# Performance work log

Hardware: AMD Instinct MI355X
Metric: run time of the kernel (lower is better)

The kernel has to match this reference:

```python
import jax, jax.numpy as jnp
import numpy as np

D_MODEL = 1024
NHEAD = 16
D_K = D_MODEL // NHEAD
EPS_ATTN = 1e-6
EPS_LN = 1e-5


def _linear(k, fan_in, fan_out):
    k1, k2 = jax.random.split(k)
    bound = 1.0 / np.sqrt(fan_in)
    W = jax.random.uniform(k1, (fan_out, fan_in), jnp.float32, -bound, bound)
    b = jax.random.uniform(k2, (fan_out,), jnp.float32, -bound, bound)
    return W, b


def setup_inputs() -> dict:
    key = jax.random.key(0)
    ks = jax.random.split(key, 8)
    src = jax.random.normal(ks[0], (4096, 4, D_MODEL), jnp.float32)
    Wq, bq = _linear(ks[1], D_MODEL, D_MODEL)
    Wk, bk = _linear(ks[2], D_MODEL, D_MODEL)
    Wv, bv = _linear(ks[3], D_MODEL, D_MODEL)
    Wo, bo = _linear(ks[4], D_MODEL, D_MODEL)
    W1, b1 = _linear(ks[5], D_MODEL, 2 * D_MODEL)
    W2, b2 = _linear(ks[6], 2 * D_MODEL, D_MODEL)
    g1 = jnp.ones((D_MODEL,), jnp.float32)
    be1 = jnp.zeros((D_MODEL,), jnp.float32)
    g2 = jnp.ones((D_MODEL,), jnp.float32)
    be2 = jnp.zeros((D_MODEL,), jnp.float32)
    return {"src": src, "Wq": Wq, "bq": bq, "Wk": Wk, "bk": bk, "Wv": Wv, "bv": bv,
            "Wo": Wo, "bo": bo, "W1": W1, "b1": b1, "W2": W2, "b2": b2,
            "g1": g1, "be1": be1, "g2": g2, "be2": be2}


def _layernorm(x, g, b):
    mu = jnp.mean(x, axis=-1, keepdims=True)
    var = jnp.mean(jnp.square(x - mu), axis=-1, keepdims=True)
    return (x - mu) * jax.lax.rsqrt(var + EPS_LN) * g + b


def reference(src, Wq, bq, Wk, bk, Wv, bv, Wo, bo, W1, b1, W2, b2, g1, be1, g2, be2):
    S, B, D = src.shape
    Q = src @ Wq.T + bq  # [S,B,D]
    K = src @ Wk.T + bk
    V = src @ Wv.T + bv
    # split heads: [S,B,H,dk]
    Q = Q.reshape(S, B, NHEAD, D_K)
    K = K.reshape(S, B, NHEAD, D_K)
    V = V.reshape(S, B, NHEAD, D_K)
    phiQ = jax.nn.elu(Q) + 1.0
    phiK = jax.nn.elu(K) + 1.0
    # context per (batch, head): [B,H,dk,dk]
    context = jnp.einsum('sbhd,sbhe->bhde', phiK, V)
    out = jnp.einsum('sbhd,bhde->sbhe', phiQ, context)
    denom = jnp.einsum('sbhd,bhd->sbh', phiQ, phiK.sum(axis=0))
    out = out / (denom[..., None] + EPS_ATTN)
    attn = out.reshape(S, B, D)  # concat heads
    out = attn @ Wo.T + bo  # dropout = identity (eval)
    out = _layernorm(src + out, g1, be1)
    ffn = jax.nn.relu(out @ W1.T + b1) @ W2.T + b2
    out = _layernorm(out + ffn, g2, be2)
    return out
```

## Files before the change

kernel.cpp:

```cpp
#include <hip/hip_runtime.h>
#include <hip/hip_bf16.h>

typedef __hip_bfloat16 bf16;
typedef __attribute__((ext_vector_type(4))) float floatx4;
typedef __attribute__((ext_vector_type(8))) short shortx8;

#define MFMA16(a, b, c) __builtin_amdgcn_mfma_f32_16x16x32_bf16(a, b, c, 0, 0, 0)

__device__ __forceinline__ void gll16(const bf16* g, void* l) {
  __builtin_amdgcn_global_load_lds((const __attribute__((address_space(1))) unsigned int*)g,
                                   (__attribute__((address_space(3))) unsigned int*)l,
                                   16, 0, 0);
}

__device__ __forceinline__ shortx8 ds8(const char* p) {
  shortx8 r;
  unsigned a = (unsigned)(unsigned long long)(const __attribute__((address_space(3))) char*)p;
  asm volatile("ds_read_b128 %0, %1" : "=v"(r) : "v"(a));
  return r;
}

__device__ __forceinline__ float b2f(short s) {
  return __bfloat162float(__builtin_bit_cast(bf16, (unsigned short)s));
}
__device__ __forceinline__ short f2b(float f) {
  return __builtin_bit_cast(short, __float2bfloat16(f));
}

__global__ __launch_bounds__(256) void f2b_all(
    const float* __restrict__ src, const float* __restrict__ Wq,
    const float* __restrict__ Wk, const float* __restrict__ Wv,
    const float* __restrict__ Wo, const float* __restrict__ W1,
    const float* __restrict__ W2, bf16* __restrict__ src_bf,
    bf16* __restrict__ Wq_b, bf16* __restrict__ Wk_b, bf16* __restrict__ Wv_b,
    bf16* __restrict__ Wo_b, bf16* __restrict__ W1_b, bf16* __restrict__ W2_b) {
  const int blk = blockIdx.x;
  const float* in;
  bf16* out;
  int off;
  if (blk < 16384)      { in = src; out = src_bf; off = blk; }
  else if (blk < 17408) { in = Wq; out = Wq_b; off = blk - 16384; }
  else if (blk < 18432) { in = Wk; out = Wk_b; off = blk - 17408; }
  else if (blk < 19456) { in = Wv; out = Wv_b; off = blk - 18432; }
  else if (blk < 20480) { in = Wo; out = Wo_b; off = blk - 19456; }
  else if (blk < 22528) { in = W1; out = W1_b; off = blk - 20480; }
  else                  { in = W2; out = W2_b; off = blk - 22528; }
  const int i = (off * 256 + threadIdx.x) * 4;
  float4 v = *(const float4*)(in + i);
  ushort4 u;
  u.x = (unsigned short)f2b(v.x);
  u.y = (unsigned short)f2b(v.y);
  u.z = (unsigned short)f2b(v.z);
  u.w = (unsigned short)f2b(v.w);
  *(ushort4*)(out + i) = u;
}

template <int EPI>
__global__ __launch_bounds__(512, 2) void gemm256(
    const bf16* __restrict__ A, const bf16* __restrict__ Bw,
    const float* __restrict__ bias0, const float* __restrict__ bias1,
    const float* __restrict__ bias2, const float* __restrict__ resf,
    const bf16* __restrict__ resb, void* __restrict__ out0,
    void* __restrict__ out1, void* __restrict__ out2, const int M,
    const int K) {
  __shared__ __align__(16) char smem[131072];
  const int tid = threadIdx.x;
  const int lane = tid & 63, wave = tid >> 6;
  const int wm = wave & 1, wn = wave >> 1;
  const int bm = blockIdx.x, bn = blockIdx.y;
  const int NK = K >> 5;

  const int srow = tid >> 2;
  const int schunk = (tid & 3) ^ ((srow >> 1) & 3);
  const bf16* gA0 = A + (size_t)(bm * 256 + srow) * K + schunk * 8;
  const bf16* gA1 = gA0 + (size_t)128 * K;
  const bf16* gB0 = Bw + (size_t)(bn * 256 + srow) * K + schunk * 8;
  const bf16* gB1 = gB0 + (size_t)128 * K;
  const unsigned ldst = (unsigned)wave * 1024u;

  const int frow = lane & 15;
  const unsigned fch16 = (unsigned)(((lane >> 4) ^ ((frow >> 1) & 3))) << 4;
  const unsigned aoff0 = (unsigned)(wm * 8192 + frow * 64) + fch16;
  const unsigned boff0 = 65536u + (unsigned)(wn * 4096 + frow * 64) + fch16;

  floatx4 acc[8][4] = {};

#define STAGE_A(t)                                                       \
  {                                                                      \
    const int kk = (t) * 32;                                             \
    const unsigned bo = (unsigned)(((t) & 3) * 16384) + ldst;            \
    gll16(gA0 + kk, smem + bo);                                          \
    gll16(gA1 + kk, smem + bo + 8192);                                   \
  }
#define STAGE_B(t)                                                       \
  {                                                                      \
    const int kk = (t) * 32;                                             \
    const unsigned bo = 65536u + (unsigned)(((t) & 3) * 16384) + ldst;   \
    gll16(gB0 + kk, smem + bo);                                          \
    gll16(gB1 + kk, smem + bo + 8192);                                   \
  }

  STAGE_A(0); STAGE_B(0);
  STAGE_A(1); STAGE_B(1);
  STAGE_A(2); STAGE_B(2);
  asm volatile("s_waitcnt vmcnt(8)");
  __builtin_amdgcn_sched_barrier(0);
  __builtin_amdgcn_s_barrier();

  for (int kt = 0; kt < NK; ++kt) {
    const unsigned ab = aoff0 + (unsigned)((kt & 3) * 16384);
    const unsigned bb = boff0 + (unsigned)((kt & 3) * 16384);
    shortx8 bfr[4], af[4];
#pragma unroll
    for (int j = 0; j < 4; j++) bfr[j] = ds8(smem + bb + j * 1024);
#pragma unroll
    for (int i2 = 0; i2 < 4; i2++) af[i2] = ds8(smem + ab + i2 * 1024);
    if (kt + 3 < NK) STAGE_A(kt + 3);
    __builtin_amdgcn_s_barrier();
    asm volatile("s_waitcnt lgkmcnt(0)");
    __builtin_amdgcn_sched_barrier(0);
    __builtin_amdgcn_s_setprio(1);
#pragma unroll
    for (int i2 = 0; i2 < 4; i2++)
#pragma unroll
      for (int j = 0; j < 4; j++) acc[i2][j] = MFMA16(af[i2], bfr[j], acc[i2][j]);
    __builtin_amdgcn_s_setprio(0);
#pragma unroll
    for (int i2 = 0; i2 < 4; i2++) af[i2] = ds8(smem + ab + (4 + i2) * 1024);
    if (kt + 3 < NK) STAGE_B(kt + 3);
    __builtin_amdgcn_s_barrier();
    asm volatile("s_waitcnt lgkmcnt(0)");
    __builtin_amdgcn_sched_barrier(0);
    __builtin_amdgcn_s_setprio(1);
#pragma unroll
    for (int i2 = 0; i2 < 4; i2++)
#pragma unroll
      for (int j = 0; j < 4; j++)
        acc[4 + i2][j] = MFMA16(af[i2], bfr[j], acc[4 + i2][j]);
    __builtin_amdgcn_s_setprio(0);
    if (kt < NK - 1) {
      if (kt < NK - 3) {
        asm volatile("s_waitcnt vmcnt(8)");
      } else if (kt == NK - 3) {
        asm volatile("s_waitcnt vmcnt(4)");
      } else {
        asm volatile("s_waitcnt vmcnt(0)");
      }
      __builtin_amdgcn_sched_barrier(0);
      __builtin_amdgcn_s_barrier();
    }
  }
#undef STAGE_A
#undef STAGE_B

  bf16* cep = (bf16*)smem;
  const float* bptr = bias0;
  bf16* ob = (bf16*)out0;
  int colbase = bn * 256;
  int phi = 0;
  if (EPI == 4) {
    const int sel = bn >> 2;
    bptr = (sel == 0) ? bias0 : (sel == 1) ? bias1 : bias2;
    ob = (bf16*)((sel == 0) ? out0 : (sel == 1) ? out1 : out2);
    colbase = (bn & 3) * 256;
    phi = (sel < 2);
  }
  const int e = lane & 15, q4 = (lane >> 4) << 2;
  float bj[4];
#pragma unroll
  for (int j = 0; j < 4; j++) bj[j] = bptr[colbase + wn * 64 + j * 16 + e];

  const int ridx = tid >> 4;
  const int cc = (tid & 15) * 8;
  const int grow_base = bm * 256 + (ridx >> 4) * 128 + (ridx & 15);

#pragma unroll
  for (int i3 = 0; i3 < 8; i3++) {
    __syncthreads();
#pragma unroll
    for (int j = 0; j < 4; j++)
#pragma unroll
      for (int r = 0; r < 4; r++) {
        float v = acc[i3][j][r] + bj[j];
        if (EPI == 4 && phi) v = v > 0.f ? v + 1.f : __expf(v);
        if (EPI == 2) v = fmaxf(v, 0.f);
        cep[(wm * 16 + q4 + r) * 268 + wn * 64 + j * 16 + e] =
            __builtin_bit_cast(bf16, f2b(v));
      }
    __syncthreads();
    const int grow = grow_base + i3 * 16;
#pragma unroll
    for (int h = 0; h < 2; h++) {
      const int col = cc + h * 128;
      shortx8 v = *(const shortx8*)&cep[ridx * 268 + col];
      if (EPI == 3) {
        const float* rp = resf + (size_t)grow * M + colbase + col;
        float4 r0 = *(const float4*)rp;
        float4 r1 = *(const float4*)(rp + 4);
        v[0] = f2b(b2f(v[0]) + r0.x); v[1] = f2b(b2f(v[1]) + r0.y);
        v[2] = f2b(b2f(v[2]) + r0.z); v[3] = f2b(b2f(v[3]) + r0.w);
        v[4] = f2b(b2f(v[4]) + r1.x); v[5] = f2b(b2f(v[5]) + r1.y);
        v[6] = f2b(b2f(v[6]) + r1.z); v[7] = f2b(b2f(v[7]) + r1.w);
      } else if (EPI == 5) {
        shortx8 rv = *(const shortx8*)(resb + (size_t)grow * M + colbase + col);
#pragma unroll
        for (int k = 0; k < 8; k++) v[k] = f2b(b2f(v[k]) + b2f(rv[k]));
      }
      *(shortx8*)(ob + (size_t)grow * M + colbase + col) = v;
    }
  }
}

__global__ __launch_bounds__(256) void ctx_mfma(const bf16* __restrict__ phiK,
                                                const bf16* __restrict__ V,
                                                float* __restrict__ ctx,
                                                float* __restrict__ ksum) {
  __shared__ __align__(16) short sKT[64][72];
  __shared__ __align__(16) short sVT[64][72];
  const int bh = blockIdx.x, b = bh >> 4, h = bh & 15;
  const int t = threadIdx.x, lane = t & 63, wave = t >> 6;
  const int s_l = t >> 2;
  const int c0 = (t & 3) << 4;
  const int frow = lane & 15, fk = (lane >> 4) << 3;
  const shortx8 ones = (shortx8)(short)0x3F80;
  floatx4 acc[4] = {};
  floatx4 accK = {};

  const int sbeg = blockIdx.y * 512;
  for (int sub = 0; sub < 8; sub++) {
    const size_t g = ((size_t)(sbeg + sub * 64 + s_l) * 4 + b) * 1024 + h * 64 + c0;
    shortx8 kv0 = *(const shortx8*)(phiK + g);
    shortx8 kv1 = *(const shortx8*)(phiK + g + 8);
    shortx8 vv0 = *(const shortx8*)(V + g);
    shortx8 vv1 = *(const shortx8*)(V + g + 8);
    __syncthreads();
#pragma unroll
    for (int j = 0; j < 8; j++) {
      sKT[c0 + j][s_l] = kv0[j];
      sKT[c0 + 8 + j][s_l] = kv1[j];
      sVT[c0 + j][s_l] = vv0[j];
      sVT[c0 + 8 + j][s_l] = vv1[j];
    }
    __syncthreads();
#pragma unroll
    for (int ks = 0; ks < 2; ks++) {
      shortx8 af = *(const shortx8*)&sKT[wave * 16 + frow][ks * 32 + fk];
      accK = MFMA16(af, ones, accK);
#pragma unroll
      for (int j = 0; j < 4; j++) {
        shortx8 bfr = *(const shortx8*)&sVT[j * 16 + frow][ks * 32 + fk];
        acc[j] = MFMA16(af, bfr, acc[j]);
      }
    }
  }

  float* cdst = ctx + (size_t)bh * 4096;
  const int dr0 = wave * 16 + ((lane >> 4) << 2);
  const int e = lane & 15;
#pragma unroll
  for (int j = 0; j < 4; j++)
#pragma unroll
    for (int r = 0; r < 4; r++)
      atomicAdd(cdst + (size_t)(dr0 + r) * 64 + j * 16 + e, acc[j][r]);
  if (e == 0) {
#pragma unroll
    for (int r = 0; r < 4; r++) atomicAdd(ksum + bh * 64 + dr0 + r, accK[r]);
  }
}

__global__ __launch_bounds__(256) void attn_mfma(const bf16* __restrict__ phiQ,
                                                 const float* __restrict__ ctx,
                                                 const float* __restrict__ ksum,
                                                 bf16* __restrict__ attn) {
  __shared__ __align__(16) bf16 sctxT[64][72];
  __shared__ __align__(16) bf16 sks[64];
  const int bh = blockIdx.x, b = bh >> 4, h = bh & 15;
  const int t = threadIdx.x, lane = t & 63, wave = t >> 6;
  const float* cbase = ctx + (size_t)bh * 4096;
  for (int idx = t; idx < 4096; idx += 256) {
    int d = idx >> 6, e = idx & 63;
    sctxT[e][d] = __float2bfloat16(cbase[idx]);
  }
  if (t < 64) sks[t] = __float2bfloat16(ksum[bh * 64 + t]);
  __syncthreads();

  const int s0 = blockIdx.y * 128 + wave * 32;
  const int frow = lane & 15, fk = (lane >> 4) << 3;
  shortx8 bfr[2][4], kfr[2];
#pragma unroll
  for (int ks = 0; ks < 2; ks++) {
#pragma unroll
    for (int j = 0; j < 4; j++) bfr[ks][j] = *(const shortx8*)&sctxT[j * 16 + frow][ks * 32 + fk];
    kfr[ks] = *(const shortx8*)&sks[ks * 32 + fk];
  }
  floatx4 acc[2][4] = {};
  floatx4 accd[2] = {};
#pragma unroll
  for (int i = 0; i < 2; i++) {
#pragma unroll
    for (int ks = 0; ks < 2; ks++) {
      const int srow = s0 + i * 16 + frow;
      const bf16* ap = phiQ + ((size_t)srow * 4 + b) * 1024 + h * 64 + ks * 32 + fk;
      shortx8 af = *(const shortx8*)ap;
#pragma unroll
      for (int j = 0; j < 4; j++) acc[i][j] = MFMA16(af, bfr[ks][j], acc[i][j]);
      accd[i] = MFMA16(af, kfr[ks], accd[i]);
    }
  }
#pragma unroll
  for (int i = 0; i < 2; i++) {
#pragma unroll
    for (int r = 0; r < 4; r++) {
      const int srow = s0 + i * 16 + ((lane >> 4) << 2) + r;
      const float den = accd[i][r] + 1e-6f;
#pragma unroll
      for (int j = 0; j < 4; j++) {
        const int e = j * 16 + (lane & 15);
        attn[((size_t)srow * 4 + b) * 1024 + h * 64 + e] = __float2bfloat16(acc[i][j][r] / den);
      }
    }
  }
}

__global__ __launch_bounds__(256) void ln_kernel(const bf16* __restrict__ x,
                                                 const float* __restrict__ g,
                                                 const float* __restrict__ be,
                                                 bf16* __restrict__ outb,
                                                 float* __restrict__ outf) {
  const int row = blockIdx.x, t = threadIdx.x;
  const ushort4 u = ((const ushort4*)(x + (size_t)row * 1024))[t];
  float v0 = b2f((short)u.x), v1 = b2f((short)u.y);
  float v2 = b2f((short)u.z), v3 = b2f((short)u.w);
  float s = v0 + v1 + v2 + v3;
  float q = v0 * v0 + v1 * v1 + v2 * v2 + v3 * v3;
#pragma unroll
  for (int off = 32; off; off >>= 1) {
    s += __shfl_xor(s, off);
    q += __shfl_xor(q, off);
  }
  __shared__ float ss[4], sq[4];
  const int wave = t >> 6;
  if ((t & 63) == 0) { ss[wave] = s; sq[wave] = q; }
  __syncthreads();
  s = ss[0] + ss[1] + ss[2] + ss[3];
  q = sq[0] + sq[1] + sq[2] + sq[3];
  const float mu = s * (1.f / 1024.f);
  const float var = q * (1.f / 1024.f) - mu * mu;
  const float rstd = rsqrtf(var + 1e-5f);
  const float4 gv = ((const float4*)g)[t];
  const float4 bv = ((const float4*)be)[t];
  float y0 = (v0 - mu) * rstd * gv.x + bv.x;
  float y1 = (v1 - mu) * rstd * gv.y + bv.y;
  float y2 = (v2 - mu) * rstd * gv.z + bv.z;
  float y3 = (v3 - mu) * rstd * gv.w + bv.w;
  if (outb != nullptr) {
    ushort4 o;
    o.x = (unsigned short)f2b(y0); o.y = (unsigned short)f2b(y1);
    o.z = (unsigned short)f2b(y2); o.w = (unsigned short)f2b(y3);
    ((ushort4*)(outb + (size_t)row * 1024))[t] = o;
  } else {
    float4 o = {y0, y1, y2, y3};
    ((float4*)(outf + (size_t)row * 1024))[t] = o;
  }
}

extern "C" void kernel_launch(void* const* d_in, const int* in_sizes, int n_in,
                              void* d_out, int out_size, void* d_ws, size_t ws_size,
                              hipStream_t stream) {
  const float* src = (const float*)d_in[0];
  const float* Wq = (const float*)d_in[1];
  const float* bq = (const float*)d_in[2];
  const float* Wk = (const float*)d_in[3];
  const float* bk = (const float*)d_in[4];
  const float* Wv = (const float*)d_in[5];
  const float* bv = (const float*)d_in[6];
  const float* Wo = (const float*)d_in[7];
  const float* bo = (const float*)d_in[8];
  const float* W1 = (const float*)d_in[9];
  const float* b1 = (const float*)d_in[10];
  const float* W2 = (const float*)d_in[11];
  const float* b2 = (const float*)d_in[12];
  const float* g1 = (const float*)d_in[13];
  const float* be1 = (const float*)d_in[14];
  const float* g2 = (const float*)d_in[15];
  const float* be2 = (const float*)d_in[16];

  const size_t MB = 1024 * 1024;
  char* w = (char*)d_ws;
  bf16* src_bf = (bf16*)(w + 0);
  bf16* x1b = (bf16*)(w + 0);
  bf16* phiQ = (bf16*)(w + 64 * MB);
  bf16* phiK = (bf16*)(w + 96 * MB);
  bf16* attn = (bf16*)(w + 96 * MB);
  bf16* Vb = (bf16*)(w + 128 * MB);
  bf16* out1b = (bf16*)(w + 128 * MB);
  bf16* x2b = (bf16*)(w + 160 * MB);
  bf16* Wq_b = (bf16*)(w + 224 * MB);
  bf16* Wk_b = (bf16*)(w + 226 * MB);
  bf16* Wv_b = (bf16*)(w + 228 * MB);
  bf16* Wo_b = (bf16*)(w + 230 * MB);
  bf16* W1_b = (bf16*)(w + 232 * MB);
  bf16* W2_b = (bf16*)(w + 236 * MB);
  float* ctx = (float*)(w + 240 * MB);
  float* ksum = (float*)(w + 241 * MB);
  bf16* H1 = (bf16*)d_out;
  float* outf = (float*)d_out;

  const dim3 blk(256), blk5(512);
  f2b_all<<<24576, blk, 0, stream>>>(src, Wq, Wk, Wv, Wo, W1, W2, src_bf, Wq_b,
                                     Wk_b, Wv_b, Wo_b, W1_b, W2_b);
  hipMemsetAsync(ctx, 0, (64 * 64 * 64 + 64 * 64) * sizeof(float), stream);

  gemm256<4><<<dim3(64, 12), blk5, 0, stream>>>(
      src_bf, Wq_b, bq, bk, bv, nullptr, nullptr, phiQ, phiK, Vb, 1024, 1024);
  ctx_mfma<<<dim3(64, 8), blk, 0, stream>>>(phiK, Vb, ctx, ksum);
  attn_mfma<<<dim3(64, 32), blk, 0, stream>>>(phiQ, ctx, ksum, attn);
  gemm256<3><<<dim3(64, 4), blk5, 0, stream>>>(
      attn, Wo_b, bo, nullptr, nullptr, src, nullptr, x1b, nullptr, nullptr, 1024, 1024);
  ln_kernel<<<16384, blk, 0, stream>>>(x1b, g1, be1, out1b, nullptr);
  gemm256<2><<<dim3(64, 8), blk5, 0, stream>>>(
      out1b, W1_b, b1, nullptr, nullptr, nullptr, nullptr, H1, nullptr, nullptr, 2048, 1024);
  gemm256<5><<<dim3(64, 4), blk5, 0, stream>>>(
      H1, W2_b, b2, nullptr, nullptr, nullptr, out1b, x2b, nullptr, nullptr, 1024, 2048);
  ln_kernel<<<16384, blk, 0, stream>>>(x2b, g2, be2, nullptr, outf);
}
```

Before: 531.8 us.

## Add double-buffered BK=64 GEMM variant for the Wo and FFN projections

Introduces a second GEMM kernel that stages 64-wide K tiles into two LDS buffers of 64KB each with XOR-swizzled chunks, using a simpler one-barrier-per-tile loop. It is used for the output projection and both FFN GEMMs, while the original multi-stage kernel (renamed) stays for the QKV projection. The aim is fewer barriers and less loop overhead per K step, at the cost of shallower prefetch depth, which may expose more global load latency.

```diff
diff --git a/kernel.cpp b/kernel.cpp
--- a/kernel.cpp
+++ b/kernel.cpp
@@ -56,7 +56,7 @@
 }
 
 template <int EPI>
-__global__ __launch_bounds__(512, 2) void gemm256(
+__global__ __launch_bounds__(512, 2) void gemm_p2(
     const bf16* __restrict__ A, const bf16* __restrict__ Bw,
     const float* __restrict__ bias0, const float* __restrict__ bias1,
     const float* __restrict__ bias2, const float* __restrict__ resf,
@@ -152,6 +152,136 @@
   }
 #undef STAGE_A
 #undef STAGE_B
+
+  bf16* cep = (bf16*)smem;
+  const float* bptr = bias0;
+  bf16* ob = (bf16*)out0;
+  int colbase = bn * 256;
+  int phi = 0;
+  if (EPI == 4) {
+    const int sel = bn >> 2;
+    bptr = (sel == 0) ? bias0 : (sel == 1) ? bias1 : bias2;
+    ob = (bf16*)((sel == 0) ? out0 : (sel == 1) ? out1 : out2);
+    colbase = (bn & 3) * 256;
+    phi = (sel < 2);
+  }
+  const int e = lane & 15, q4 = (lane >> 4) << 2;
+  float bj[4];
+#pragma unroll
+  for (int j = 0; j < 4; j++) bj[j] = bptr[colbase + wn * 64 + j * 16 + e];
+
+  const int ridx = tid >> 4;
+  const int cc = (tid & 15) * 8;
+  const int grow_base = bm * 256 + (ridx >> 4) * 128 + (ridx & 15);
+
+#pragma unroll
+  for (int i3 = 0; i3 < 8; i3++) {
+    __syncthreads();
+#pragma unroll
+    for (int j = 0; j < 4; j++)
+#pragma unroll
+      for (int r = 0; r < 4; r++) {
+        float v = acc[i3][j][r] + bj[j];
+        if (EPI == 4 && phi) v = v > 0.f ? v + 1.f : __expf(v);
+        if (EPI == 2) v = fmaxf(v, 0.f);
+        cep[(wm * 16 + q4 + r) * 268 + wn * 64 + j * 16 + e] =
+            __builtin_bit_cast(bf16, f2b(v));
+      }
+    __syncthreads();
+    const int grow = grow_base + i3 * 16;
+#pragma unroll
+    for (int h = 0; h < 2; h++) {
+      const int col = cc + h * 128;
+      shortx8 v = *(const shortx8*)&cep[ridx * 268 + col];
+      if (EPI == 3) {
+        const float* rp = resf + (size_t)grow * M + colbase + col;
+        float4 r0 = *(const float4*)rp;
+        float4 r1 = *(const float4*)(rp + 4);
+        v[0] = f2b(b2f(v[0]) + r0.x); v[1] = f2b(b2f(v[1]) + r0.y);
+        v[2] = f2b(b2f(v[2]) + r0.z); v[3] = f2b(b2f(v[3]) + r0.w);
+        v[4] = f2b(b2f(v[4]) + r1.x); v[5] = f2b(b2f(v[5]) + r1.y);
+        v[6] = f2b(b2f(v[6]) + r1.z); v[7] = f2b(b2f(v[7]) + r1.w);
+      } else if (EPI == 5) {
+        shortx8 rv = *(const shortx8*)(resb + (size_t)grow * M + colbase + col);
+#pragma unroll
+        for (int k = 0; k < 8; k++) v[k] = f2b(b2f(v[k]) + b2f(rv[k]));
+      }
+      *(shortx8*)(ob + (size_t)grow * M + colbase + col) = v;
+    }
+  }
+}
+
+template <int EPI>
+__global__ __launch_bounds__(512, 2) void gemm_mb(
+    const bf16* __restrict__ A, const bf16* __restrict__ Bw,
+    const float* __restrict__ bias0, const float* __restrict__ bias1,
+    const float* __restrict__ bias2, const float* __restrict__ resf,
+    const bf16* __restrict__ resb, void* __restrict__ out0,
+    void* __restrict__ out1, void* __restrict__ out2, const int M,
+    const int K) {
+  __shared__ __align__(16) char smem[131072];
+  const int tid = threadIdx.x;
+  const int lane = tid & 63, wave = tid >> 6;
+  const int wm = wave & 1, wn = wave >> 1;
+  const int bm = blockIdx.x, bn = blockIdx.y;
+  const int NT = K >> 6;
+
+  const int srow = tid >> 3;
+  const int sch = (tid & 7) ^ (srow & 7);
+  const bf16* gA0 = A + (size_t)(bm * 256 + srow) * K + sch * 8;
+  const bf16* gB0 = Bw + (size_t)(bn * 256 + srow) * K + sch * 8;
+  const unsigned ldst = (unsigned)wave * 1024u;
+
+  const int frow = lane & 15, lq = lane >> 4, x7 = frow & 7;
+  const unsigned arow = (unsigned)(wm * 128 + frow) * 128u;
+  const unsigned brow = 32768u + (unsigned)(wn * 64 + frow) * 128u;
+  const unsigned aoffA = arow + (unsigned)((lq ^ x7) * 16);
+  const unsigned aoffB = arow + (unsigned)(((4 | lq) ^ x7) * 16);
+  const unsigned boffA = brow + (unsigned)((lq ^ x7) * 16);
+  const unsigned boffB = brow + (unsigned)(((4 | lq) ^ x7) * 16);
+
+  floatx4 acc[8][4] = {};
+
+#define STAGE(t)                                                           \
+  {                                                                        \
+    const int kk = (t) * 64;                                               \
+    const unsigned so2 = (unsigned)(((t) & 1) * 65536);                    \
+    gll16(gA0 + kk, smem + so2 + ldst);                                    \
+    gll16(gA0 + (size_t)64 * K + kk, smem + so2 + 8192 + ldst);            \
+    gll16(gA0 + (size_t)128 * K + kk, smem + so2 + 16384 + ldst);          \
+    gll16(gA0 + (size_t)192 * K + kk, smem + so2 + 24576 + ldst);          \
+    gll16(gB0 + kk, smem + so2 + 32768 + ldst);                            \
+    gll16(gB0 + (size_t)64 * K + kk, smem + so2 + 40960 + ldst);           \
+    gll16(gB0 + (size_t)128 * K + kk, smem + so2 + 49152 + ldst);          \
+    gll16(gB0 + (size_t)192 * K + kk, smem + so2 + 57344 + ldst);          \
+  }
+
+  STAGE(0);
+  __syncthreads();
+
+  for (int kt = 0; kt < NT; ++kt) {
+    const unsigned so = (unsigned)((kt & 1) * 65536);
+    if (kt + 1 < NT) STAGE(kt + 1);
+    shortx8 af[8], bfr[4];
+#pragma unroll
+    for (int ks = 0; ks < 2; ks++) {
+      const unsigned ao = so + (ks ? aoffB : aoffA);
+      const unsigned bo = so + (ks ? boffB : boffA);
+#pragma unroll
+      for (int j = 0; j < 4; j++)
+        bfr[j] = *(const shortx8*)(smem + bo + j * 2048);
+#pragma unroll
+      for (int i = 0; i < 8; i++)
+        af[i] = *(const shortx8*)(smem + ao + i * 2048);
+#pragma unroll
+      for (int i = 0; i < 8; i++)
+#pragma unroll
+        for (int j = 0; j < 4; j++)
+          acc[i][j] = MFMA16(af[i], bfr[j], acc[i][j]);
+    }
+    __syncthreads();
+  }
+#undef STAGE
 
   bf16* cep = (bf16*)smem;
   const float* bptr = bias0;
@@ -411,16 +541,16 @@
                                      Wk_b, Wv_b, Wo_b, W1_b, W2_b);
   hipMemsetAsync(ctx, 0, (64 * 64 * 64 + 64 * 64) * sizeof(float), stream);
 
-  gemm256<4><<<dim3(64, 12), blk5, 0, stream>>>(
+  gemm_p2<4><<<dim3(64, 12), blk5, 0, stream>>>(
       src_bf, Wq_b, bq, bk, bv, nullptr, nullptr, phiQ, phiK, Vb, 1024, 1024);
   ctx_mfma<<<dim3(64, 8), blk, 0, stream>>>(phiK, Vb, ctx, ksum);
   attn_mfma<<<dim3(64, 32), blk, 0, stream>>>(phiQ, ctx, ksum, attn);
-  gemm256<3><<<dim3(64, 4), blk5, 0, stream>>>(
+  gemm_mb<3><<<dim3(64, 4), blk5, 0, stream>>>(
       attn, Wo_b, bo, nullptr, nullptr, src, nullptr, x1b, nullptr, nullptr, 1024, 1024);
   ln_kernel<<<16384, blk, 0, stream>>>(x1b, g1, be1, out1b, nullptr);
-  gemm256<2><<<dim3(64, 8), blk5, 0, stream>>>(
+  gemm_mb<2><<<dim3(64, 8), blk5, 0, stream>>>(
       out1b, W1_b, b1, nullptr, nullptr, nullptr, nullptr, H1, nullptr, nullptr, 2048, 1024);
-  gemm256<5><<<dim3(64, 4), blk5, 0, stream>>>(
+  gemm_mb<5><<<dim3(64, 4), blk5, 0, stream>>>(
       H1, W2_b, b2, nullptr, nullptr, nullptr, out1b, x2b, nullptr, nullptr, 1024, 2048);
   ln_kernel<<<16384, blk, 0, stream>>>(x2b, g2, be2, nullptr, outf);
 }
```

New measurement: 516.3 us. -2.9%, faster.
